# Optimization experiments

Measured on AMD Instinct MI355X. Metric: run time of the kernel, lower is better.

## Reference

```python
import jax, jax.numpy as jnp
import numpy as np

# Module config (matches init_kwargs)
W_BIT = 2
PS_BIT = 8
IC = 256
OC = 256
K = 3
N_XBAR = 576
STRIDE = 1
PAD = 1
NUM_IC = min(IC, N_XBAR // (K * K))   # 64 input channels per crossbar array
GROUPS = IC // NUM_IC                 # 4 arrays (col_slide), ic divides evenly
QP_W = 2 ** W_BIT - 1                 # unsigned levels for nonneg pos/neg weights
QN_PS = -(2 ** (PS_BIT - 1))          # signed psum range
QP_PS = 2 ** (PS_BIT - 1) - 1


def lsq(v, s, qn, qp):
    """LSQ quantize-dequantize with straight-through rounding."""
    vs = jnp.clip(v / s, qn, qp)
    vbar = vs + jax.lax.stop_gradient(jnp.round(vs) - vs)
    return vbar * s


def conv2d(x, w):
    # x: [B, C, H, W], w: [O, C, k, k]
    return jax.lax.conv_general_dilated(
        x, w, window_strides=(STRIDE, STRIDE),
        padding=((PAD, PAD), (PAD, PAD)),
        dimension_numbers=('NCHW', 'OIHW', 'NCHW'))


def setup_inputs() -> dict:
    key = jax.random.key(0)
    k1, k2, k3, k4, k5 = jax.random.split(key, 5)
    x = jax.random.normal(k1, (16, IC, 56, 56), dtype=jnp.float32)
    weight = jax.random.normal(k2, (OC, IC, K, K), dtype=jnp.float32) * 0.05
    # positive LSQ step sizes, roughly 2*E|w|/sqrt(Qp) scale
    w_scale = jax.random.uniform(k3, (GROUPS,), dtype=jnp.float32) * 0.04 + 0.01
    ps_scale_p = jax.random.uniform(k4, (GROUPS,), dtype=jnp.float32) * 0.05 + 0.02
    ps_scale_n = jax.random.uniform(k5, (GROUPS,), dtype=jnp.float32) * 0.05 + 0.02
    return {"x": x, "weight": weight, "w_scale": w_scale,
            "ps_scale_p": ps_scale_p, "ps_scale_n": ps_scale_n}


def reference(x, weight, w_scale, ps_scale_p, ps_scale_n):
    B, _, H, W = x.shape
    # im2col tiling over input channels into GROUPS crossbar arrays
    xg = x.reshape(B, GROUPS, NUM_IC, H, W)                  # [B,G,cg,H,W]
    wg = weight.reshape(OC, GROUPS, NUM_IC, K, K)            # [O,G,cg,k,k]
    # pos / neg weight split, per-array LSQ weight quantization (shared quantizer)
    s_w = w_scale[:, None, None, None, None]                 # [G,1,1,1,1]
    wg_t = jnp.transpose(wg, (1, 0, 2, 3, 4))                # [G,O,cg,k,k]
    wq_p = lsq(jax.nn.relu(wg_t), s_w, 0, QP_W)
    wq_n = lsq(jax.nn.relu(-wg_t), s_w, 0, QP_W)
    xg_t = jnp.transpose(xg, (1, 0, 2, 3, 4))                # [G,B,cg,H,W]
    # per-array partial-sum convs (vmapped over arrays)
    vconv = jax.vmap(conv2d, in_axes=(0, 0))
    psum_p = vconv(xg_t, wq_p)                               # [G,B,O,h,w]
    psum_n = vconv(xg_t, wq_n)
    # per-array psum LSQ quantization ('Array' mode), then accumulate
    s_p = ps_scale_p[:, None, None, None, None]
    s_n = ps_scale_n[:, None, None, None, None]
    out_p = jnp.sum(lsq(psum_p, s_p, QN_PS, QP_PS), axis=0)  # [B,O,h,w]
    out_n = jnp.sum(lsq(psum_n, s_n, QN_PS, QP_PS), axis=0)
    return out_p - out_n
```

## Files before the change

kernel.cpp:

```cpp
#include <hip/hip_runtime.h>
#include <hip/hip_bf16.h>

typedef __attribute__((ext_vector_type(8))) short bf16x8_t;
typedef __attribute__((ext_vector_type(4))) float f32x4_t;

#define XP_BYTES 55115776u
#define WT_BYTES 2359296u

typedef __attribute__((address_space(1))) const unsigned int ga_u32_t;
typedef __attribute__((address_space(3))) unsigned int lds_u32_t;

__device__ __forceinline__ void g2l16(const void* g, void* l) {
  __builtin_amdgcn_global_load_lds((ga_u32_t*)g, (lds_u32_t*)l, 16, 0, 0);
}

__global__ __launch_bounds__(256) void prep_x(const float* __restrict__ x,
                                              __hip_bfloat16* __restrict__ xp) {
  __shared__ float ls[64 * 57];
  int blk = blockIdx.x;
  int g = blk / 896;
  int r = blk - g * 896;
  int b = r / 56;
  int h = r - b * 56;
  int tid = threadIdx.x;
  const float* src = x + (size_t)(b * 256 + g * 64) * 3136 + h * 56;
  for (int i = tid; i < 64 * 56; i += 256) {
    int c = i / 56, w = i - c * 56;
    ls[c * 57 + w] = src[(size_t)c * 3136 + w];
  }
  __syncthreads();
  __hip_bfloat16* dst = xp + ((size_t)((g * 16 + b) * 58 + h + 1) * 58 + 1) * 128;
  int wp = tid >> 7;
  int inner = tid & 127;
  int hl = inner >> 6, c = inner & 63;
  for (int w0 = 0; w0 < 56; w0 += 2) {
    int w = w0 + wp;
    float v = ls[c * 57 + w];
    __hip_bfloat16 hi = __float2bfloat16(v);
    __hip_bfloat16 val = hl ? __float2bfloat16(v - __bfloat162float(hi)) : hi;
    dst[(size_t)w * 128 + inner] = val;
  }
}

__global__ __launch_bounds__(256) void prep_w(const float* __restrict__ wgt,
                                              const float* __restrict__ wsc,
                                              __hip_bfloat16* __restrict__ wt) {
  int idx = blockIdx.x * 256 + threadIdx.x;
  if (idx >= 589824) return;
  int oc = idx / 2304;
  int r = idx - oc * 2304;
  int C = r / 9;
  int tap = r - C * 9;
  int g = C >> 6, c = C & 63;
  float s = wsc[g];
  float rv = wgt[idx] / s;
  float ip = rintf(fminf(fmaxf(rv, 0.f), 3.f));
  float iN = rintf(fminf(fmaxf(-rv, 0.f), 3.f));
  size_t base_p = (size_t)((g * 2 + 0) * 256 + oc) * 576 + tap * 64 + c;
  size_t base_n = (size_t)((g * 2 + 1) * 256 + oc) * 576 + tap * 64 + c;
  wt[base_p] = __float2bfloat16(ip);
  wt[base_n] = __float2bfloat16(iN);
}

#define MEMPIN asm volatile("" ::: "memory")
#define BAR __builtin_amdgcn_s_barrier()
#define VMCNT0 asm volatile("s_waitcnt vmcnt(0)" ::: "memory")

__global__ __launch_bounds__(256, 2) void conv_mfma(
    const unsigned short* __restrict__ xp, const unsigned short* __restrict__ wt,
    const float* __restrict__ wsc, const float* __restrict__ psp,
    const float* __restrict__ psn, float* __restrict__ out) {
  __shared__ char Astrip[65536];
  __shared__ char Bbuf[16384];

  const int bid = blockIdx.x;
  const int wg = (bid & 7) * 98 + (bid >> 3);
  const int b = wg / 49;
  const int t = wg - b * 49;
  const int r0 = (t << 6) / 56;

  const int tid = threadIdx.x;
  const int wv = tid >> 6;
  const int l = tid & 63;

  int pxb[4];
#pragma unroll
  for (int mi = 0; mi < 4; ++mi) {
    int m = (t << 6) + mi * 16 + (l & 15);
    int rv = m / 56, w = m - rv * 56;
    pxb[mi] = ((rv - r0) << 6) + w;
  }
  int boffr[4];
#pragma unroll
  for (int ni = 0; ni < 4; ++ni) {
    int row = (wv << 6) + ni * 16 + (l & 15);
    boffr[ni] = (row << 6) + (((l >> 4) ^ ((row >> 1) & 3)) << 4);
  }

  float w0s = wsc[0], w1s = wsc[1], w2s = wsc[2], w3s = wsc[3];
  float p0 = psp[0], p1 = psp[1], p2 = psp[2], p3 = psp[3];
  float n0 = psn[0], n1 = psn[1], n2 = psn[2], n3 = psn[3];

  f32x4_t acc[4][4], oacc[4][4];
  const f32x4_t fz = {0.f, 0.f, 0.f, 0.f};
#pragma unroll
  for (int i = 0; i < 4; ++i)
#pragma unroll
    for (int j = 0; j < 4; ++j) { acc[i][j] = fz; oacc[i][j] = fz; }

  const char* xg = (const char*)xp;
  const char* wgp = (const char*)wt;
  const unsigned a_gbbase = (unsigned)((b * 3364 + r0 * 58) * 256);

#define STAGE_STRIP(gg)                                                        \
  {                                                                            \
    const char* s_ = xg + (unsigned)(gg)*13778944u + a_gbbase;                 \
    _Pragma("unroll")                                                          \
    for (int k_ = 0; k_ < 16; ++k_) {                                          \
      int idx_ = tid + (k_ << 8);                                              \
      int px_ = idx_ >> 4, sl_ = idx_ & 15;                                    \
      int sr_ = px_ >> 6, xc_ = px_ & 63;                                      \
      g2l16(s_ + (sr_ * 58 + xc_) * 256 +                                      \
                (((sl_ & 8) | ((sl_ & 7) ^ (xc_ & 7))) << 4),                  \
            Astrip + idx_ * 16);                                               \
    }                                                                          \
  }

#define STAGE_B(uu)                                                            \
  {                                                                            \
    const int u_ = (uu);                                                       \
    const int g_ = u_ / 36;                                                    \
    const int r_ = u_ - g_ * 36;                                               \
    const int sg_ = (r_ >= 18) ? 1 : 0;                                        \
    const int r18_ = r_ - (sg_ ? 18 : 0);                                      \
    const char* s_ = wgp + (size_t)((g_ * 2 + sg_) * 256) * 1152 +             \
                     (r18_ >> 1) * 128 + (r18_ & 1) * 64;                      \
    _Pragma("unroll")                                                          \
    for (int k_ = 0; k_ < 4; ++k_) {                                           \
      int idx_ = tid + (k_ << 8);                                              \
      int row_ = idx_ >> 2, sl_ = idx_ & 3;                                    \
      g2l16(s_ + row_ * 1152 + ((sl_ ^ ((row_ >> 1) & 3)) << 4),               \
            Bbuf + idx_ * 16);                                                 \
    }                                                                          \
  }

  STAGE_STRIP(0);
  STAGE_B(0);

  for (int u = 0; u < 144; ++u) {
    const int g = u / 36;
    const int r36 = u - g * 36;
    const int sgn = (r36 >= 18) ? 1 : 0;
    const int r18 = r36 - (sgn ? 18 : 0);
    const int tap = r18 >> 1, cc = r18 & 1;
    const int ty = tap / 3, tx = tap - ty * 3;
    const int tapoff = (ty << 6) + tx;

    VMCNT0;
    BAR;
    MEMPIN;

    bf16x8_t ahi[4], alo[4], bfr[4];
    const int kj = (cc << 2) + (l >> 4);
#pragma unroll
    for (int mi = 0; mi < 4; ++mi) {
      int px = pxb[mi] + tapoff;
      int base = (px << 8) + ((kj ^ (px & 7)) << 4);
      ahi[mi] = *(const bf16x8_t*)(Astrip + base);
      alo[mi] = *(const bf16x8_t*)(Astrip + base + 128);
    }
#pragma unroll
    for (int ni = 0; ni < 4; ++ni)
      bfr[ni] = *(const bf16x8_t*)(Bbuf + boffr[ni]);
    MEMPIN;
    BAR;
    MEMPIN;

    if (r36 == 35 && u < 143) { STAGE_STRIP(g + 1); }
    if (u + 1 < 144) { STAGE_B(u + 1); }

    __builtin_amdgcn_s_setprio(1);
#pragma unroll
    for (int mi = 0; mi < 4; ++mi)
#pragma unroll
      for (int ni = 0; ni < 4; ++ni) {
        acc[mi][ni] = __builtin_amdgcn_mfma_f32_16x16x32_bf16(ahi[mi], bfr[ni], acc[mi][ni], 0, 0, 0);
        acc[mi][ni] = __builtin_amdgcn_mfma_f32_16x16x32_bf16(alo[mi], bfr[ni], acc[mi][ni], 0, 0, 0);
      }
    __builtin_amdgcn_s_setprio(0);

    if (r36 == 17 || r36 == 35) {
      float sw = (g & 2) ? ((g & 1) ? w3s : w2s) : ((g & 1) ? w1s : w0s);
      float sp = (g & 2) ? ((g & 1) ? p3 : p2) : ((g & 1) ? p1 : p0);
      float sn = (g & 2) ? ((g & 1) ? n3 : n2) : ((g & 1) ? n1 : n0);
      float sq = sgn ? sn : sp;
      float rs = sw / sq;
      float sgnmul = sgn ? -sq : sq;
#pragma unroll
      for (int mi = 0; mi < 4; ++mi)
#pragma unroll
        for (int ni = 0; ni < 4; ++ni)
#pragma unroll
          for (int j = 0; j < 4; ++j) {
            float v = acc[mi][ni][j] * rs;
            v = fminf(fmaxf(v, -128.f), 127.f);
            oacc[mi][ni][j] += sgnmul * rintf(v);
            acc[mi][ni][j] = 0.f;
          }
    }
  }

#pragma unroll
  for (int ni = 0; ni < 4; ++ni) {
    int oc = (wv << 6) + ni * 16 + (l & 15);
    float* orow = out + ((size_t)(b * 256 + oc)) * 3136;
#pragma unroll
    for (int mi = 0; mi < 4; ++mi) {
      int m0 = (t << 6) + mi * 16 + ((l >> 4) << 2);
#pragma unroll
      for (int j = 0; j < 4; ++j) {
        orow[m0 + j] = oacc[mi][ni][j];
      }
    }
  }
#undef STAGE_STRIP
#undef STAGE_B
}

__global__ __launch_bounds__(256) void naive_conv(
    const float* __restrict__ x, const float* __restrict__ wgt,
    const float* __restrict__ wsc, const float* __restrict__ psp,
    const float* __restrict__ psn, float* __restrict__ out) {
  int idx = blockIdx.x * 256 + threadIdx.x;
  if (idx >= 12845056) return;
  int b = idx / 802816;
  int r = idx - b * 802816;
  int oc = r / 3136;
  int hw = r - oc * 3136;
  int h = hw / 56, w = hw - (hw / 56) * 56;
  float o = 0.f;
  for (int g = 0; g < 4; ++g) {
    float sw = wsc[g];
    float inv = 1.f / sw;
    float pp = 0.f, pn = 0.f;
    for (int tap = 0; tap < 9; ++tap) {
      int y = h + tap / 3 - 1, xx = w + tap % 3 - 1;
      if (y < 0 || y > 55 || xx < 0 || xx > 55) continue;
      const float* xr = x + (size_t)(b * 256 + g * 64) * 3136 + y * 56 + xx;
      const float* wrr = wgt + (size_t)oc * 2304 + (size_t)(g * 64) * 9 + tap;
      for (int c = 0; c < 64; ++c) {
        float xv = xr[(size_t)c * 3136];
        float rv = wrr[c * 9] * inv;
        pp += xv * rintf(fminf(fmaxf(rv, 0.f), 3.f));
        pn += xv * rintf(fminf(fmaxf(-rv, 0.f), 3.f));
      }
    }
    float sp = psp[g], sn = psn[g];
    o += rintf(fminf(fmaxf(pp * (sw / sp), -128.f), 127.f)) * sp;
    o -= rintf(fminf(fmaxf(pn * (sw / sn), -128.f), 127.f)) * sn;
  }
  out[idx] = o;
}

extern "C" void kernel_launch(void* const* d_in, const int* in_sizes, int n_in,
                              void* d_out, int out_size, void* d_ws, size_t ws_size,
                              hipStream_t stream) {
  const float* x = (const float*)d_in[0];
  const float* wgt = (const float*)d_in[1];
  const float* wsc = (const float*)d_in[2];
  const float* psp = (const float*)d_in[3];
  const float* psn = (const float*)d_in[4];
  float* out = (float*)d_out;

  if (ws_size >= (size_t)XP_BYTES + (size_t)WT_BYTES) {
    unsigned short* xpw = (unsigned short*)d_ws;
    unsigned short* wtw = (unsigned short*)((char*)d_ws + XP_BYTES);
    hipMemsetAsync(d_ws, 0, XP_BYTES, stream);
    prep_x<<<3584, 256, 0, stream>>>(x, (__hip_bfloat16*)xpw);
    prep_w<<<2304, 256, 0, stream>>>(wgt, wsc, (__hip_bfloat16*)wtw);
    conv_mfma<<<784, 256, 0, stream>>>(xpw, wtw, wsc, psp, psn, out);
  } else {
    naive_conv<<<(12845056 + 255) / 256, 256, 0, stream>>>(x, wgt, wsc, psp, psn, out);
  }
}
```

Measured before the change: 288.0 us.

## Use 512-thread blocks with 2x4 wave tiling and triple-buffered weight staging

The conv kernel moves to 512 threads per block, laid out as a 2x4 grid of waves, so each wave computes a 32x64 tile instead of 64x64. Weight tiles are now triple-buffered in LDS and prefetched two steps ahead, waiting on vmcnt(2) instead of vmcnt(0). This removes one barrier per iteration except at group boundaries, where the input strip is restaged. The aim is more waves to hide latency and less stall from barriers and loads, at the cost of more LDS per block and fewer MFMAs per A-fragment load.

Measured after the change: 391.3 us. 35.9% more time.

```diff
diff --git a/kernel.cpp b/kernel.cpp
--- a/kernel.cpp
+++ b/kernel.cpp
@@ -64,14 +64,18 @@
 
 #define MEMPIN asm volatile("" ::: "memory")
 #define BAR __builtin_amdgcn_s_barrier()
+#define VMCNT2 asm volatile("s_waitcnt vmcnt(2)" ::: "memory")
 #define VMCNT0 asm volatile("s_waitcnt vmcnt(0)" ::: "memory")
-
-__global__ __launch_bounds__(256, 2) void conv_mfma(
+#define LGKM0_FENCE                                   \
+  asm volatile("s_waitcnt lgkmcnt(0)" ::: "memory");  \
+  __builtin_amdgcn_sched_barrier(0)
+
+__global__ __launch_bounds__(512, 1) void conv_mfma(
     const unsigned short* __restrict__ xp, const unsigned short* __restrict__ wt,
     const float* __restrict__ wsc, const float* __restrict__ psp,
     const float* __restrict__ psn, float* __restrict__ out) {
   __shared__ char Astrip[65536];
-  __shared__ char Bbuf[16384];
+  __shared__ char Bbuf[49152];
 
   const int bid = blockIdx.x;
   const int wg = (bid & 7) * 98 + (bid >> 3);
@@ -82,18 +86,19 @@
   const int tid = threadIdx.x;
   const int wv = tid >> 6;
   const int l = tid & 63;
-
-  int pxb[4];
-#pragma unroll
-  for (int mi = 0; mi < 4; ++mi) {
-    int m = (t << 6) + mi * 16 + (l & 15);
+  const int wr = wv >> 2, wc = wv & 3;
+
+  int pxb[2];
+#pragma unroll
+  for (int mi = 0; mi < 2; ++mi) {
+    int m = (t << 6) + wr * 32 + mi * 16 + (l & 15);
     int rv = m / 56, w = m - rv * 56;
     pxb[mi] = ((rv - r0) << 6) + w;
   }
   int boffr[4];
 #pragma unroll
   for (int ni = 0; ni < 4; ++ni) {
-    int row = (wv << 6) + ni * 16 + (l & 15);
+    int row = (wc << 6) + ni * 16 + (l & 15);
     boffr[ni] = (row << 6) + (((l >> 4) ^ ((row >> 1) & 3)) << 4);
   }
 
@@ -101,10 +106,10 @@
   float p0 = psp[0], p1 = psp[1], p2 = psp[2], p3 = psp[3];
   float n0 = psn[0], n1 = psn[1], n2 = psn[2], n3 = psn[3];
 
-  f32x4_t acc[4][4], oacc[4][4];
+  f32x4_t acc[2][4], oacc[2][4];
   const f32x4_t fz = {0.f, 0.f, 0.f, 0.f};
 #pragma unroll
-  for (int i = 0; i < 4; ++i)
+  for (int i = 0; i < 2; ++i)
 #pragma unroll
     for (int j = 0; j < 4; ++j) { acc[i][j] = fz; oacc[i][j] = fz; }
 
@@ -116,8 +121,8 @@
   {                                                                            \
     const char* s_ = xg + (unsigned)(gg)*13778944u + a_gbbase;                 \
     _Pragma("unroll")                                                          \
-    for (int k_ = 0; k_ < 16; ++k_) {                                          \
-      int idx_ = tid + (k_ << 8);                                              \
+    for (int k_ = 0; k_ < 8; ++k_) {                                           \
+      int idx_ = tid + (k_ << 9);                                              \
       int px_ = idx_ >> 4, sl_ = idx_ & 15;                                    \
       int sr_ = px_ >> 6, xc_ = px_ & 63;                                      \
       g2l16(s_ + (sr_ * 58 + xc_) * 256 +                                      \
@@ -135,17 +140,19 @@
     const int r18_ = r_ - (sg_ ? 18 : 0);                                      \
     const char* s_ = wgp + (size_t)((g_ * 2 + sg_) * 256) * 1152 +             \
                      (r18_ >> 1) * 128 + (r18_ & 1) * 64;                      \
+    char* d_ = Bbuf + (u_ % 3) * 16384;                                        \
     _Pragma("unroll")                                                          \
-    for (int k_ = 0; k_ < 4; ++k_) {                                           \
-      int idx_ = tid + (k_ << 8);                                              \
+    for (int k_ = 0; k_ < 2; ++k_) {                                           \
+      int idx_ = tid + (k_ << 9);                                              \
       int row_ = idx_ >> 2, sl_ = idx_ & 3;                                    \
       g2l16(s_ + row_ * 1152 + ((sl_ ^ ((row_ >> 1) & 3)) << 4),               \
-            Bbuf + idx_ * 16);                                                 \
+            d_ + idx_ * 16);                                                   \
     }                                                                          \
   }
 
   STAGE_STRIP(0);
   STAGE_B(0);
+  STAGE_B(1);
 
   for (int u = 0; u < 144; ++u) {
     const int g = u / 36;
@@ -156,14 +163,15 @@
     const int ty = tap / 3, tx = tap - ty * 3;
     const int tapoff = (ty << 6) + tx;
 
-    VMCNT0;
+    if (u == 143) { VMCNT0; } else { VMCNT2; }
     BAR;
     MEMPIN;
 
-    bf16x8_t ahi[4], alo[4], bfr[4];
+    const char* bb = Bbuf + (u % 3) * 16384;
+    bf16x8_t ahi[2], alo[2], bfr[4];
     const int kj = (cc << 2) + (l >> 4);
 #pragma unroll
-    for (int mi = 0; mi < 4; ++mi) {
+    for (int mi = 0; mi < 2; ++mi) {
       int px = pxb[mi] + tapoff;
       int base = (px << 8) + ((kj ^ (px & 7)) << 4);
       ahi[mi] = *(const bf16x8_t*)(Astrip + base);
@@ -171,17 +179,24 @@
     }
 #pragma unroll
     for (int ni = 0; ni < 4; ++ni)
-      bfr[ni] = *(const bf16x8_t*)(Bbuf + boffr[ni]);
+      bfr[ni] = *(const bf16x8_t*)(bb + boffr[ni]);
     MEMPIN;
-    BAR;
-    MEMPIN;
-
-    if (r36 == 35 && u < 143) { STAGE_STRIP(g + 1); }
-    if (u + 1 < 144) { STAGE_B(u + 1); }
+
+    if (r36 == 35) {
+      if (u < 143) {
+        LGKM0_FENCE;
+        BAR;
+        MEMPIN;
+        STAGE_STRIP(g + 1);
+        STAGE_B(u + 2);
+      }
+    } else if (u + 2 < 144) {
+      STAGE_B(u + 2);
+    }
 
     __builtin_amdgcn_s_setprio(1);
 #pragma unroll
-    for (int mi = 0; mi < 4; ++mi)
+    for (int mi = 0; mi < 2; ++mi)
 #pragma unroll
       for (int ni = 0; ni < 4; ++ni) {
         acc[mi][ni] = __builtin_amdgcn_mfma_f32_16x16x32_bf16(ahi[mi], bfr[ni], acc[mi][ni], 0, 0, 0);
@@ -197,7 +212,7 @@
       float rs = sw / sq;
       float sgnmul = sgn ? -sq : sq;
 #pragma unroll
-      for (int mi = 0; mi < 4; ++mi)
+      for (int mi = 0; mi < 2; ++mi)
 #pragma unroll
         for (int ni = 0; ni < 4; ++ni)
 #pragma unroll
@@ -212,11 +227,11 @@
 
 #pragma unroll
   for (int ni = 0; ni < 4; ++ni) {
-    int oc = (wv << 6) + ni * 16 + (l & 15);
+    int oc = (wc << 6) + ni * 16 + (l & 15);
     float* orow = out + ((size_t)(b * 256 + oc)) * 3136;
 #pragma unroll
-    for (int mi = 0; mi < 4; ++mi) {
-      int m0 = (t << 6) + mi * 16 + ((l >> 4) << 2);
+    for (int mi = 0; mi < 2; ++mi) {
+      int m0 = (t << 6) + wr * 32 + mi * 16 + ((l >> 4) << 2);
 #pragma unroll
       for (int j = 0; j < 4; ++j) {
         orow[m0 + j] = oacc[mi][ni][j];
@@ -278,7 +293,7 @@
     hipMemsetAsync(d_ws, 0, XP_BYTES, stream);
     prep_x<<<3584, 256, 0, stream>>>(x, (__hip_bfloat16*)xpw);
     prep_w<<<2304, 256, 0, stream>>>(wgt, wsc, (__hip_bfloat16*)wtw);
-    conv_mfma<<<784, 256, 0, stream>>>(xpw, wtw, wsc, psp, psn, out);
+    conv_mfma<<<784, 512, 0, stream>>>(xpw, wtw, wsc, psp, psn, out);
   } else {
     naive_conv<<<(12845056 + 255) / 256, 256, 0, stream>>>(x, wgt, wsc, psp, psn, out);
   }
```

## Load MFMA B fragments directly to registers with double-buffered prefetch, drop B LDS

Applied to the files above, without the earlier changes.

prep_w now writes the quantized weights pre-swizzled into per-lane MFMA fragment order, so each wave loads its B operands straight from global memory into registers and the LDS B buffer goes away. The main loop handles two K-chunks per iteration with register double buffering (bA/bB), waits with vmcnt(4), and only barriers at strip restage points rather than twice per step. This aims to remove per-step LDS traffic and barrier stalls, at the cost of more VGPRs and global/L2 reads of weights by every block.

Result: faster. 249.5 us (-13.4%).

```diff
diff --git a/kernel.cpp b/kernel.cpp
--- a/kernel.cpp
+++ b/kernel.cpp
@@ -3,6 +3,7 @@
 
 typedef __attribute__((ext_vector_type(8))) short bf16x8_t;
 typedef __attribute__((ext_vector_type(4))) float f32x4_t;
+typedef __attribute__((ext_vector_type(4))) unsigned int u32x4_t;
 
 #define XP_BYTES 55115776u
 #define WT_BYTES 2359296u
@@ -44,34 +45,49 @@
 
 __global__ __launch_bounds__(256) void prep_w(const float* __restrict__ wgt,
                                               const float* __restrict__ wsc,
-                                              __hip_bfloat16* __restrict__ wt) {
+                                              unsigned short* __restrict__ wtf) {
   int idx = blockIdx.x * 256 + threadIdx.x;
-  if (idx >= 589824) return;
-  int oc = idx / 2304;
-  int r = idx - oc * 2304;
-  int C = r / 9;
-  int tap = r - C * 9;
-  int g = C >> 6, c = C & 63;
-  float s = wsc[g];
-  float rv = wgt[idx] / s;
-  float ip = rintf(fminf(fmaxf(rv, 0.f), 3.f));
-  float iN = rintf(fminf(fmaxf(-rv, 0.f), 3.f));
-  size_t base_p = (size_t)((g * 2 + 0) * 256 + oc) * 576 + tap * 64 + c;
-  size_t base_n = (size_t)((g * 2 + 1) * 256 + oc) * 576 + tap * 64 + c;
-  wt[base_p] = __float2bfloat16(ip);
-  wt[base_n] = __float2bfloat16(iN);
+  if (idx >= 147456) return;
+  int l = idx & 63;
+  int ni = (idx >> 6) & 3;
+  int wq = (idx >> 8) & 3;
+  int u = idx >> 10;
+  int g = u / 36;
+  int r36 = u - g * 36;
+  int sgn = (r36 >= 18) ? 1 : 0;
+  int r18 = r36 - sgn * 18;
+  int tap = r18 >> 1, cc = r18 & 1;
+  int oc = wq * 64 + ni * 16 + (l & 15);
+  float inv = 1.f / wsc[g];
+  unsigned short pk[8];
+#pragma unroll
+  for (int e = 0; e < 8; ++e) {
+    int c = cc * 32 + ((l >> 4) << 3) + e;
+    float w = wgt[(size_t)oc * 2304 + (g * 64 + c) * 9 + tap] * inv;
+    if (sgn) w = -w;
+    float q = rintf(fminf(fmaxf(w, 0.f), 3.f));
+    union { __hip_bfloat16 h; unsigned short s; } cv;
+    cv.h = __float2bfloat16(q);
+    pk[e] = cv.s;
+  }
+  u32x4_t v;
+  v[0] = (unsigned)pk[0] | ((unsigned)pk[1] << 16);
+  v[1] = (unsigned)pk[2] | ((unsigned)pk[3] << 16);
+  v[2] = (unsigned)pk[4] | ((unsigned)pk[5] << 16);
+  v[3] = (unsigned)pk[6] | ((unsigned)pk[7] << 16);
+  *(u32x4_t*)(wtf + (size_t)idx * 8) = v;
 }
 
 #define MEMPIN asm volatile("" ::: "memory")
 #define BAR __builtin_amdgcn_s_barrier()
+#define VMCNT4 asm volatile("s_waitcnt vmcnt(4)" ::: "memory")
 #define VMCNT0 asm volatile("s_waitcnt vmcnt(0)" ::: "memory")
 
 __global__ __launch_bounds__(256, 2) void conv_mfma(
-    const unsigned short* __restrict__ xp, const unsigned short* __restrict__ wt,
+    const unsigned short* __restrict__ xp, const unsigned short* __restrict__ wtf,
     const float* __restrict__ wsc, const float* __restrict__ psp,
     const float* __restrict__ psn, float* __restrict__ out) {
   __shared__ char Astrip[65536];
-  __shared__ char Bbuf[16384];
 
   const int bid = blockIdx.x;
   const int wg = (bid & 7) * 98 + (bid >> 3);
@@ -90,12 +106,6 @@
     int rv = m / 56, w = m - rv * 56;
     pxb[mi] = ((rv - r0) << 6) + w;
   }
-  int boffr[4];
-#pragma unroll
-  for (int ni = 0; ni < 4; ++ni) {
-    int row = (wv << 6) + ni * 16 + (l & 15);
-    boffr[ni] = (row << 6) + (((l >> 4) ^ ((row >> 1) & 3)) << 4);
-  }
 
   float w0s = wsc[0], w1s = wsc[1], w2s = wsc[2], w3s = wsc[3];
   float p0 = psp[0], p1 = psp[1], p2 = psp[2], p3 = psp[3];
@@ -109,7 +119,7 @@
     for (int j = 0; j < 4; ++j) { acc[i][j] = fz; oacc[i][j] = fz; }
 
   const char* xg = (const char*)xp;
-  const char* wgp = (const char*)wt;
+  const char* wtb = (const char*)wtf + (wv << 12) + (l << 4);
   const unsigned a_gbbase = (unsigned)((b * 3364 + r0 * 58) * 256);
 
 #define STAGE_STRIP(gg)                                                        \
@@ -126,88 +136,100 @@
     }                                                                          \
   }
 
-#define STAGE_B(uu)                                                            \
+#define LOADB(d0, d1, d2, d3, uu)                                              \
   {                                                                            \
-    const int u_ = (uu);                                                       \
-    const int g_ = u_ / 36;                                                    \
-    const int r_ = u_ - g_ * 36;                                               \
-    const int sg_ = (r_ >= 18) ? 1 : 0;                                        \
-    const int r18_ = r_ - (sg_ ? 18 : 0);                                      \
-    const char* s_ = wgp + (size_t)((g_ * 2 + sg_) * 256) * 1152 +             \
-                     (r18_ >> 1) * 128 + (r18_ & 1) * 64;                      \
+    const char* p_ = wtb + (unsigned)(uu) * 16384u;                            \
+    d0 = *(const bf16x8_t*)(p_);                                               \
+    d1 = *(const bf16x8_t*)(p_ + 1024);                                        \
+    d2 = *(const bf16x8_t*)(p_ + 2048);                                        \
+    d3 = *(const bf16x8_t*)(p_ + 3072);                                        \
+  }
+
+#define READA(cc_, tyo_)                                                       \
+  {                                                                            \
+    const int kj_ = ((cc_) << 2) + (l >> 4);                                   \
     _Pragma("unroll")                                                          \
-    for (int k_ = 0; k_ < 4; ++k_) {                                           \
-      int idx_ = tid + (k_ << 8);                                              \
-      int row_ = idx_ >> 2, sl_ = idx_ & 3;                                    \
-      g2l16(s_ + row_ * 1152 + ((sl_ ^ ((row_ >> 1) & 3)) << 4),               \
-            Bbuf + idx_ * 16);                                                 \
+    for (int mi = 0; mi < 4; ++mi) {                                           \
+      int px_ = pxb[mi] + (tyo_);                                              \
+      int base_ = (px_ << 8) + ((kj_ ^ (px_ & 7)) << 4);                       \
+      ahi[mi] = *(const bf16x8_t*)(Astrip + base_);                            \
+      alo[mi] = *(const bf16x8_t*)(Astrip + base_ + 128);                      \
     }                                                                          \
   }
 
+#define MMA32(B0, B1, B2, B3)                                                  \
+  __builtin_amdgcn_s_setprio(1);                                               \
+  _Pragma("unroll")                                                            \
+  for (int mi = 0; mi < 4; ++mi) {                                             \
+    acc[mi][0] = __builtin_amdgcn_mfma_f32_16x16x32_bf16(ahi[mi], B0, acc[mi][0], 0, 0, 0); \
+    acc[mi][1] = __builtin_amdgcn_mfma_f32_16x16x32_bf16(ahi[mi], B1, acc[mi][1], 0, 0, 0); \
+    acc[mi][2] = __builtin_amdgcn_mfma_f32_16x16x32_bf16(ahi[mi], B2, acc[mi][2], 0, 0, 0); \
+    acc[mi][3] = __builtin_amdgcn_mfma_f32_16x16x32_bf16(ahi[mi], B3, acc[mi][3], 0, 0, 0); \
+    acc[mi][0] = __builtin_amdgcn_mfma_f32_16x16x32_bf16(alo[mi], B0, acc[mi][0], 0, 0, 0); \
+    acc[mi][1] = __builtin_amdgcn_mfma_f32_16x16x32_bf16(alo[mi], B1, acc[mi][1], 0, 0, 0); \
+    acc[mi][2] = __builtin_amdgcn_mfma_f32_16x16x32_bf16(alo[mi], B2, acc[mi][2], 0, 0, 0); \
+    acc[mi][3] = __builtin_amdgcn_mfma_f32_16x16x32_bf16(alo[mi], B3, acc[mi][3], 0, 0, 0); \
+  }                                                                            \
+  __builtin_amdgcn_s_setprio(0);
+
+#define QUANTIZE(gg, ss)                                                       \
+  {                                                                            \
+    float sw = ((gg) & 2) ? (((gg) & 1) ? w3s : w2s) : (((gg) & 1) ? w1s : w0s); \
+    float sp = ((gg) & 2) ? (((gg) & 1) ? p3 : p2) : (((gg) & 1) ? p1 : p0);   \
+    float sn = ((gg) & 2) ? (((gg) & 1) ? n3 : n2) : (((gg) & 1) ? n1 : n0);   \
+    float sq = (ss) ? sn : sp;                                                 \
+    float rs = sw / sq;                                                        \
+    float sm = (ss) ? -sq : sq;                                                \
+    _Pragma("unroll")                                                          \
+    for (int mi = 0; mi < 4; ++mi)                                             \
+      _Pragma("unroll")                                                        \
+      for (int ni = 0; ni < 4; ++ni)                                           \
+        _Pragma("unroll")                                                      \
+        for (int j = 0; j < 4; ++j) {                                          \
+          float v = acc[mi][ni][j] * rs;                                       \
+          v = fminf(fmaxf(v, -128.f), 127.f);                                  \
+          oacc[mi][ni][j] += sm * rintf(v);                                    \
+          acc[mi][ni][j] = 0.f;                                                \
+        }                                                                      \
+  }
+
+  bf16x8_t ahi[4], alo[4];
+  bf16x8_t bA0, bA1, bA2, bA3, bB0, bB1, bB2, bB3;
+
   STAGE_STRIP(0);
-  STAGE_B(0);
-
-  for (int u = 0; u < 144; ++u) {
-    const int g = u / 36;
-    const int r36 = u - g * 36;
-    const int sgn = (r36 >= 18) ? 1 : 0;
-    const int r18 = r36 - (sgn ? 18 : 0);
-    const int tap = r18 >> 1, cc = r18 & 1;
-    const int ty = tap / 3, tx = tap - ty * 3;
-    const int tapoff = (ty << 6) + tx;
-
-    VMCNT0;
-    BAR;
+  MEMPIN;
+  LOADB(bA0, bA1, bA2, bA3, 0);
+  LOADB(bB0, bB1, bB2, bB3, 1);
+
+  int tap = 0, sgn = 0, g = 0;
+  for (int v = 0; v < 72; ++v) {
+    const int ty = tap / 3;
+    const int tyo = (ty << 6) + (tap - ty * 3);
+
+    VMCNT4;
+    if (tap == 0) { BAR; }
     MEMPIN;
-
-    bf16x8_t ahi[4], alo[4], bfr[4];
-    const int kj = (cc << 2) + (l >> 4);
-#pragma unroll
-    for (int mi = 0; mi < 4; ++mi) {
-      int px = pxb[mi] + tapoff;
-      int base = (px << 8) + ((kj ^ (px & 7)) << 4);
-      ahi[mi] = *(const bf16x8_t*)(Astrip + base);
-      alo[mi] = *(const bf16x8_t*)(Astrip + base + 128);
+    READA(0, tyo);
+    MMA32(bA0, bA1, bA2, bA3);
+    MEMPIN;
+    if (v < 71) { LOADB(bA0, bA1, bA2, bA3, 2 * v + 2); }
+
+    if (v == 71) { VMCNT0; } else { VMCNT4; }
+    MEMPIN;
+    READA(1, tyo);
+    MMA32(bB0, bB1, bB2, bB3);
+
+    if (tap == 8) {
+      QUANTIZE(g, sgn);
+      if (sgn == 1 && v < 71) {
+        BAR;
+        STAGE_STRIP(g + 1);
+      }
     }
-#pragma unroll
-    for (int ni = 0; ni < 4; ++ni)
-      bfr[ni] = *(const bf16x8_t*)(Bbuf + boffr[ni]);
     MEMPIN;
-    BAR;
-    MEMPIN;
-
-    if (r36 == 35 && u < 143) { STAGE_STRIP(g + 1); }
-    if (u + 1 < 144) { STAGE_B(u + 1); }
-
-    __builtin_amdgcn_s_setprio(1);
-#pragma unroll
-    for (int mi = 0; mi < 4; ++mi)
-#pragma unroll
-      for (int ni = 0; ni < 4; ++ni) {
-        acc[mi][ni] = __builtin_amdgcn_mfma_f32_16x16x32_bf16(ahi[mi], bfr[ni], acc[mi][ni], 0, 0, 0);
-        acc[mi][ni] = __builtin_amdgcn_mfma_f32_16x16x32_bf16(alo[mi], bfr[ni], acc[mi][ni], 0, 0, 0);
-      }
-    __builtin_amdgcn_s_setprio(0);
-
-    if (r36 == 17 || r36 == 35) {
-      float sw = (g & 2) ? ((g & 1) ? w3s : w2s) : ((g & 1) ? w1s : w0s);
-      float sp = (g & 2) ? ((g & 1) ? p3 : p2) : ((g & 1) ? p1 : p0);
-      float sn = (g & 2) ? ((g & 1) ? n3 : n2) : ((g & 1) ? n1 : n0);
-      float sq = sgn ? sn : sp;
-      float rs = sw / sq;
-      float sgnmul = sgn ? -sq : sq;
-#pragma unroll
-      for (int mi = 0; mi < 4; ++mi)
-#pragma unroll
-        for (int ni = 0; ni < 4; ++ni)
-#pragma unroll
-          for (int j = 0; j < 4; ++j) {
-            float v = acc[mi][ni][j] * rs;
-            v = fminf(fmaxf(v, -128.f), 127.f);
-            oacc[mi][ni][j] += sgnmul * rintf(v);
-            acc[mi][ni][j] = 0.f;
-          }
-    }
+    if (v < 71) { LOADB(bB0, bB1, bB2, bB3, 2 * v + 3); }
+
+    if (++tap == 9) { tap = 0; g += sgn; sgn ^= 1; }
   }
 
 #pragma unroll
@@ -224,7 +246,10 @@
     }
   }
 #undef STAGE_STRIP
-#undef STAGE_B
+#undef LOADB
+#undef READA
+#undef MMA32
+#undef QUANTIZE
 }
 
 __global__ __launch_bounds__(256) void naive_conv(
@@ -277,7 +302,7 @@
     unsigned short* wtw = (unsigned short*)((char*)d_ws + XP_BYTES);
     hipMemsetAsync(d_ws, 0, XP_BYTES, stream);
     prep_x<<<3584, 256, 0, stream>>>(x, (__hip_bfloat16*)xpw);
-    prep_w<<<2304, 256, 0, stream>>>(wgt, wsc, (__hip_bfloat16*)wtw);
+    prep_w<<<576, 256, 0, stream>>>(wgt, wsc, wtw);
     conv_mfma<<<784, 256, 0, stream>>>(xpw, wtw, wsc, psp, psn, out);
   } else {
     naive_conv<<<(12845056 + 255) / 256, 256, 0, stream>>>(x, wgt, wsc, psp, psn, out);
```
